# Optimization experiments

Hardware: AMD Instinct MI355X
Metric: run time of the kernel (lower is better)

Reference implementation:

```python
import jax, jax.numpy as jnp
import numpy as np

K = 2  # number of propagation hops (SGConv K)
NEG_SLOPE = 0.1


def setup_inputs() -> dict:
    key = jax.random.key(0)
    k1, k2, k3, k4 = jax.random.split(key, 4)
    N, E, C_in, C_out = 50000, 800000, 128, 512
    x = jax.random.normal(k1, (N, C_in), dtype=jnp.float32)
    edge_index = jax.random.randint(k2, (2, E), 0, N, dtype=jnp.int64)
    W = jax.random.normal(k3, (C_out, C_in), dtype=jnp.float32) * (1.0 / np.sqrt(C_in))
    b = jax.random.normal(k4, (C_out,), dtype=jnp.float32) * 0.01
    return {"x": x, "edge_index": edge_index, "W": W, "b": b}


def reference(x, edge_index, W, b):
    N = x.shape[0]
    # gcn_norm with self-loops (PyG SGConv default: add_self_loops=True)
    loop = jnp.arange(N, dtype=edge_index.dtype)
    src = jnp.concatenate([edge_index[0], loop])  # message sources j
    dst = jnp.concatenate([edge_index[1], loop])  # aggregation targets i
    deg = jax.ops.segment_sum(jnp.ones_like(dst, dtype=x.dtype), dst, num_segments=N)
    dinv = jnp.where(deg > 0, jax.lax.rsqrt(deg), 0.0)
    norm = dinv[src] * dinv[dst]  # [E+N]
    h = x
    for _ in range(K):
        h = jax.ops.segment_sum(norm[:, None] * h[src], dst, num_segments=N)
    y = h @ W.T + b
    return jnp.where(y >= 0, y, NEG_SLOPE * y)  # LeakyReLU(0.1)
```

## Files before the change

### kernel.cpp

```cpp
#include <hip/hip_runtime.h>
#include <hip/hip_bf16.h>

#define CIN 128
#define COUT 512
#define NEG_SLOPE 0.1f

typedef __bf16 bf16x8 __attribute__((ext_vector_type(8)));
typedef float f32x4 __attribute__((ext_vector_type(4)));

static __device__ __forceinline__ unsigned short f2bf(float f) {
  unsigned int u = __builtin_bit_cast(unsigned int, f);
  unsigned int lsb = (u >> 16) & 1u;
  u += 0x7fffu + lsb;
  return (unsigned short)(u >> 16);
}
static __device__ __forceinline__ float bf_lo(unsigned int u) {
  return __builtin_bit_cast(float, u << 16);
}
static __device__ __forceinline__ float bf_hi(unsigned int u) {
  return __builtin_bit_cast(float, u & 0xffff0000u);
}
static __device__ __forceinline__ unsigned int pack2(float lo, float hi) {
  return (unsigned int)f2bf(lo) | ((unsigned int)f2bf(hi) << 16);
}

__global__ void decode_count_kernel(const int* __restrict__ raw,
                                    int* __restrict__ srcA, int* __restrict__ dstA,
                                    int* __restrict__ rank, int* __restrict__ cnt,
                                    int E, int N) {
  __shared__ int s_is32;
  if (threadIdx.x == 0) s_is32 = 0;
  __syncthreads();
  int e = blockIdx.x * blockDim.x + threadIdx.x;
  int probe = 0;
  if (e < E) probe = raw[2 * e + 1];
  if (probe != 0) s_is32 = 1;
  __syncthreads();
  if (e >= E) return;
  int s, d;
  if (!s_is32) {
    int2 sv = ((const int2*)raw)[e];
    int2 dv = ((const int2*)raw)[E + e];
    s = sv.x;
    d = dv.x;
  } else {
    s = raw[e];
    d = raw[E + e];
  }
  if ((unsigned)s >= (unsigned)N) s = 0;
  if ((unsigned)d >= (unsigned)N) d = 0;
  srcA[e] = s;
  dstA[e] = d;
  rank[e] = atomicAdd(&cnt[d], 1);
}

__global__ __launch_bounds__(256) void scan_kernel(const int* __restrict__ cnt,
                                                   int* __restrict__ rowptr,
                                                   int* __restrict__ gcur, int N) {
  __shared__ int buf[256];
  __shared__ int sbase;
  int tid = threadIdx.x;
  int base = blockIdx.x * 1024 + tid * 4;
  int v[4];
  int tot = 0;
#pragma unroll
  for (int k = 0; k < 4; ++k) {
    int i = base + k;
    v[k] = (i < N) ? cnt[i] : 0;
    tot += v[k];
  }
  buf[tid] = tot;
  __syncthreads();
  for (int off = 1; off < 256; off <<= 1) {
    int t = (tid >= off) ? buf[tid - off] : 0;
    __syncthreads();
    buf[tid] += t;
    __syncthreads();
  }
  if (tid == 255) sbase = atomicAdd(gcur, buf[255]);
  __syncthreads();
  int run = sbase + buf[tid] - tot;
#pragma unroll
  for (int k = 0; k < 4; ++k) {
    int i = base + k;
    if (i < N) rowptr[i] = run;
    run += v[k];
  }
}

__global__ __launch_bounds__(256) void scatter_prep_kernel(
    const int* __restrict__ srcA, const int* __restrict__ dstA,
    const int* __restrict__ rank, const int* __restrict__ rowptr,
    int* __restrict__ col, int E,
    const float* __restrict__ x, const int* __restrict__ cnt,
    unsigned short* __restrict__ xs,
    const float* __restrict__ W, unsigned short* __restrict__ Wbf, int N) {
  int idx = blockIdx.x * blockDim.x + threadIdx.x;
  if (idx < E) {
    int d = dstA[idx];
    col[rowptr[d] + rank[idx]] = srcA[idx];
  }
  int nx = N * (CIN / 4);
  if (idx < nx) {
    int row = idx >> 5;
    float d = 1.0f / sqrtf((float)(cnt[row] + 1));
    float4 v = ((const float4*)x)[idx];
    ushort4 o;
    o.x = f2bf(v.x * d); o.y = f2bf(v.y * d); o.z = f2bf(v.z * d); o.w = f2bf(v.w * d);
    ((ushort4*)xs)[idx] = o;
  } else {
    int t = idx - nx;
    if (t < (COUT * CIN / 8)) {
      int lane = t & 63;
      int kk = (t >> 6) & 3;
      int nt = (t >> 8) & 7;
      int wv = t >> 11;
      int row = wv * 128 + nt * 16 + (lane & 15);
      int c = kk * 32 + (lane >> 4) * 8;
      const float* src = W + (size_t)row * CIN + c;
      float4 v0 = *(const float4*)src;
      float4 v1 = *(const float4*)(src + 4);
      ushort4 o0, o1;
      o0.x = f2bf(v0.x); o0.y = f2bf(v0.y); o0.z = f2bf(v0.z); o0.w = f2bf(v0.w);
      o1.x = f2bf(v1.x); o1.y = f2bf(v1.y); o1.z = f2bf(v1.z); o1.w = f2bf(v1.w);
      ((ushort4*)Wbf)[2 * t] = o0;
      ((ushort4*)Wbf)[2 * t + 1] = o1;
    }
  }
}

template <bool SQ>
__global__ __launch_bounds__(256) void hop_kernel(
    const unsigned short* __restrict__ Xs,
    const int* __restrict__ rowptr, const int* __restrict__ cnt,
    const int* __restrict__ col, unsigned short* __restrict__ Y, int N) {
  int lane = threadIdx.x & 63;
  int wid = threadIdx.x >> 6;
  int node = blockIdx.x * 4 + wid;
  if (node >= N) return;
  int sub = lane & 15;
  int grp = lane >> 4;
  int beg = rowptr[node];
  int num = cnt[node];
  const uint4* X4 = (const uint4*)Xs;
  float acc[8] = {0.f, 0.f, 0.f, 0.f, 0.f, 0.f, 0.f, 0.f};
  if (grp == 0) {
    uint4 s = X4[(size_t)node * 16 + sub];
    acc[0] = bf_lo(s.x); acc[1] = bf_hi(s.x);
    acc[2] = bf_lo(s.y); acc[3] = bf_hi(s.y);
    acc[4] = bf_lo(s.z); acc[5] = bf_hi(s.z);
    acc[6] = bf_lo(s.w); acc[7] = bf_hi(s.w);
  }
  const int* cp = col + beg;
  int kb = 0;
  for (; kb + 16 <= num; kb += 16) {
    int j0 = cp[kb + grp];
    int j1 = cp[kb + 4 + grp];
    int j2 = cp[kb + 8 + grp];
    int j3 = cp[kb + 12 + grp];
    uint4 v0 = X4[(size_t)j0 * 16 + sub];
    uint4 v1 = X4[(size_t)j1 * 16 + sub];
    uint4 v2 = X4[(size_t)j2 * 16 + sub];
    uint4 v3 = X4[(size_t)j3 * 16 + sub];
    acc[0] += bf_lo(v0.x); acc[1] += bf_hi(v0.x);
    acc[2] += bf_lo(v0.y); acc[3] += bf_hi(v0.y);
    acc[4] += bf_lo(v0.z); acc[5] += bf_hi(v0.z);
    acc[6] += bf_lo(v0.w); acc[7] += bf_hi(v0.w);
    acc[0] += bf_lo(v1.x); acc[1] += bf_hi(v1.x);
    acc[2] += bf_lo(v1.y); acc[3] += bf_hi(v1.y);
    acc[4] += bf_lo(v1.z); acc[5] += bf_hi(v1.z);
    acc[6] += bf_lo(v1.w); acc[7] += bf_hi(v1.w);
    acc[0] += bf_lo(v2.x); acc[1] += bf_hi(v2.x);
    acc[2] += bf_lo(v2.y); acc[3] += bf_hi(v2.y);
    acc[4] += bf_lo(v2.z); acc[5] += bf_hi(v2.z);
    acc[6] += bf_lo(v2.w); acc[7] += bf_hi(v2.w);
    acc[0] += bf_lo(v3.x); acc[1] += bf_hi(v3.x);
    acc[2] += bf_lo(v3.y); acc[3] += bf_hi(v3.y);
    acc[4] += bf_lo(v3.z); acc[5] += bf_hi(v3.z);
    acc[6] += bf_lo(v3.w); acc[7] += bf_hi(v3.w);
  }
  int rem = num - kb;
  if (rem >= 8) {
    int j0 = cp[kb + grp];
    int j1 = cp[kb + 4 + grp];
    uint4 v0 = X4[(size_t)j0 * 16 + sub];
    uint4 v1 = X4[(size_t)j1 * 16 + sub];
    acc[0] += bf_lo(v0.x); acc[1] += bf_hi(v0.x);
    acc[2] += bf_lo(v0.y); acc[3] += bf_hi(v0.y);
    acc[4] += bf_lo(v0.z); acc[5] += bf_hi(v0.z);
    acc[6] += bf_lo(v0.w); acc[7] += bf_hi(v0.w);
    acc[0] += bf_lo(v1.x); acc[1] += bf_hi(v1.x);
    acc[2] += bf_lo(v1.y); acc[3] += bf_hi(v1.y);
    acc[4] += bf_lo(v1.z); acc[5] += bf_hi(v1.z);
    acc[6] += bf_lo(v1.w); acc[7] += bf_hi(v1.w);
    kb += 8; rem -= 8;
  }
  if (rem >= 4) {
    int j0 = cp[kb + grp];
    uint4 v0 = X4[(size_t)j0 * 16 + sub];
    acc[0] += bf_lo(v0.x); acc[1] += bf_hi(v0.x);
    acc[2] += bf_lo(v0.y); acc[3] += bf_hi(v0.y);
    acc[4] += bf_lo(v0.z); acc[5] += bf_hi(v0.z);
    acc[6] += bf_lo(v0.w); acc[7] += bf_hi(v0.w);
    kb += 4; rem -= 4;
  }
  if (grp < rem) {
    int j0 = cp[kb + grp];
    uint4 v0 = X4[(size_t)j0 * 16 + sub];
    acc[0] += bf_lo(v0.x); acc[1] += bf_hi(v0.x);
    acc[2] += bf_lo(v0.y); acc[3] += bf_hi(v0.y);
    acc[4] += bf_lo(v0.z); acc[5] += bf_hi(v0.z);
    acc[6] += bf_lo(v0.w); acc[7] += bf_hi(v0.w);
  }
#pragma unroll
  for (int r = 0; r < 8; ++r) acc[r] += __shfl_xor(acc[r], 16, 64);
#pragma unroll
  for (int r = 0; r < 8; ++r) acc[r] += __shfl_xor(acc[r], 32, 64);
  if (grp == 0) {
    float di = 1.0f / sqrtf((float)(num + 1));
    float sc = SQ ? di * di : di;
    uint4 o;
    o.x = pack2(acc[0] * sc, acc[1] * sc);
    o.y = pack2(acc[2] * sc, acc[3] * sc);
    o.z = pack2(acc[4] * sc, acc[5] * sc);
    o.w = pack2(acc[6] * sc, acc[7] * sc);
    ((uint4*)Y)[(size_t)node * 16 + sub] = o;
  }
}

__global__ __launch_bounds__(256) void gemm_kernel(
    const unsigned short* __restrict__ Abf, const unsigned short* __restrict__ Wbf,
    const float* __restrict__ bias, float* __restrict__ out, int M) {
  __shared__ float tile[16 * 516];
  int wave = threadIdx.x >> 6;
  int lane = threadIdx.x & 63;
  int quad = lane >> 4;
  int l16 = lane & 15;
  int mbase = blockIdx.x * 32;

  int m0 = mbase + l16;
  int m1 = mbase + 16 + l16;
  bool v0 = m0 < M;
  bool v1 = m1 < M;

  bf16x8 af[2][4];
#pragma unroll
  for (int kk = 0; kk < 4; ++kk) {
    af[0][kk] = v0 ? *(const bf16x8*)(Abf + (size_t)m0 * CIN + kk * 32 + quad * 8) : bf16x8{};
    af[1][kk] = v1 ? *(const bf16x8*)(Abf + (size_t)m1 * CIN + kk * 32 + quad * 8) : bf16x8{};
  }

  const bf16x8* Wf = (const bf16x8*)Wbf;
  int nbase = wave * 128;
  f32x4 acc0[8], acc1[8];
#pragma unroll
  for (int nt = 0; nt < 8; ++nt) {
    bf16x8 wf[4];
#pragma unroll
    for (int kk = 0; kk < 4; ++kk)
      wf[kk] = Wf[(((wave * 8 + nt) * 4 + kk) << 6) + lane];
    f32x4 a0 = {}, a1 = {};
#pragma unroll
    for (int kk = 0; kk < 4; ++kk) {
      a0 = __builtin_amdgcn_mfma_f32_16x16x32_bf16(wf[kk], af[0][kk], a0, 0, 0, 0);
      a1 = __builtin_amdgcn_mfma_f32_16x16x32_bf16(wf[kk], af[1][kk], a1, 0, 0, 0);
    }
    acc0[nt] = a0;
    acc1[nt] = a1;
  }

#pragma unroll
  for (int half = 0; half < 2; ++half) {
    if (half) __syncthreads();
#pragma unroll
    for (int nt = 0; nt < 8; ++nt) {
      int n0 = nbase + nt * 16 + quad * 4;
      float4 bv = *(const float4*)(bias + n0);
      f32x4 a = half ? acc1[nt] : acc0[nt];
      float4 o;
      o.x = a[0] + bv.x; o.x = (o.x >= 0.f) ? o.x : NEG_SLOPE * o.x;
      o.y = a[1] + bv.y; o.y = (o.y >= 0.f) ? o.y : NEG_SLOPE * o.y;
      o.z = a[2] + bv.z; o.z = (o.z >= 0.f) ? o.z : NEG_SLOPE * o.z;
      o.w = a[3] + bv.w; o.w = (o.w >= 0.f) ? o.w : NEG_SLOPE * o.w;
      *(float4*)&tile[l16 * 516 + n0] = o;
    }
    __syncthreads();
#pragma unroll
    for (int it = 0; it < 8; ++it) {
      int r = it * 2 + (threadIdx.x >> 7);
      int c = (threadIdx.x & 127) * 4;
      int m = mbase + half * 16 + r;
      if (m < M) *(float4*)(out + (size_t)m * COUT + c) = *(const float4*)&tile[r * 516 + c];
    }
  }
}

static inline size_t align_up(size_t v, size_t a) { return (v + a - 1) & ~(a - 1); }

extern "C" void kernel_launch(void* const* d_in, const int* in_sizes, int n_in,
                              void* d_out, int out_size, void* d_ws, size_t ws_size,
                              hipStream_t stream) {
  const float* x = (const float*)d_in[0];
  const int* edge_raw = (const int*)d_in[1];
  const float* W = (const float*)d_in[2];
  const float* b = (const float*)d_in[3];
  float* out = (float*)d_out;

  const int N = in_sizes[0] / CIN;
  const int E = in_sizes[1] / 2;
  const int NB = (N + 1023) / 1024;

  char* w = (char*)d_ws;
  int* gcur = (int*)w;            w += 256;
  int* cnt = (int*)w;             w += align_up((size_t)N * 4, 256);
  int* rowptr = (int*)w;          w += align_up((size_t)N * 4, 256);
  int* srcA = (int*)w;            w += align_up((size_t)E * 4, 256);
  int* dstA = (int*)w;            w += align_up((size_t)E * 4, 256);
  int* rank = (int*)w;            w += align_up((size_t)E * 4, 256);
  int* col = (int*)w;             w += align_up((size_t)E * 4, 256);
  unsigned short* h2bf = (unsigned short*)w;  w += align_up((size_t)N * CIN * 2, 256);
  unsigned short* Wbf = (unsigned short*)w;   w += align_up((size_t)COUT * CIN * 2, 256);

  size_t outb = (size_t)out_size * sizeof(float);
  size_t rowb = (size_t)N * CIN * sizeof(unsigned short);
  unsigned short* h1s = (unsigned short*)((char*)d_out + (outb - rowb));
  unsigned short* xs = (unsigned short*)((char*)d_out + (outb - 2 * rowb));

  hipMemsetAsync(gcur, 0, 256 + (size_t)N * sizeof(int), stream);

  decode_count_kernel<<<(E + 255) / 256, 256, 0, stream>>>(edge_raw, srcA, dstA, rank, cnt, E, N);
  scan_kernel<<<NB, 256, 0, stream>>>(cnt, rowptr, gcur, N);

  int prep_elems = N * (CIN / 4) + COUT * CIN / 8;
  int sp_threads = (E > prep_elems) ? E : prep_elems;
  scatter_prep_kernel<<<(sp_threads + 255) / 256, 256, 0, stream>>>(
      srcA, dstA, rank, rowptr, col, E, x, cnt, xs, W, Wbf, N);

  hop_kernel<true><<<(N + 3) / 4, 256, 0, stream>>>(xs, rowptr, cnt, col, h1s, N);
  hop_kernel<false><<<(N + 3) / 4, 256, 0, stream>>>(h1s, rowptr, cnt, col, h2bf, N);

  gemm_kernel<<<(N + 31) / 32, 256, 0, stream>>>(h2bf, Wbf, b, out, N);
}
```

Baseline: 266.0 us.

## Fuse second propagation hop into GEMM kernel via shared-memory tile

The second SpMM hop now runs inside the GEMM kernel. Each block aggregates its 32 destination rows into a shared-memory bf16 tile, then feeds that tile straight to the MFMA loop. This drops one kernel launch and the write and re-read of the h2 intermediate in global memory. In exchange each GEMM block runs a serial gather over 8 nodes per wave before its matrix work, with fewer blocks (N/32) in flight for the gather phase, and h1 moves from the output buffer into workspace.

```diff
diff --git a/kernel.cpp b/kernel.cpp
--- a/kernel.cpp
+++ b/kernel.cpp
@@ -129,8 +129,7 @@
   }
 }
 
-template <bool SQ>
-__global__ __launch_bounds__(256) void hop_kernel(
+__global__ __launch_bounds__(256) void hop1_kernel(
     const unsigned short* __restrict__ Xs,
     const int* __restrict__ rowptr, const int* __restrict__ cnt,
     const int* __restrict__ col, unsigned short* __restrict__ Y, int N) {
@@ -218,7 +217,7 @@
   for (int r = 0; r < 8; ++r) acc[r] += __shfl_xor(acc[r], 32, 64);
   if (grp == 0) {
     float di = 1.0f / sqrtf((float)(num + 1));
-    float sc = SQ ? di * di : di;
+    float sc = di * di;
     uint4 o;
     o.x = pack2(acc[0] * sc, acc[1] * sc);
     o.y = pack2(acc[2] * sc, acc[3] * sc);
@@ -228,26 +227,122 @@
   }
 }
 
-__global__ __launch_bounds__(256) void gemm_kernel(
-    const unsigned short* __restrict__ Abf, const unsigned short* __restrict__ Wbf,
-    const float* __restrict__ bias, float* __restrict__ out, int M) {
-  __shared__ float tile[16 * 516];
+__global__ __launch_bounds__(256) void hopgemm_kernel(
+    const unsigned short* __restrict__ Xs,
+    const int* __restrict__ rowptr, const int* __restrict__ cnt,
+    const int* __restrict__ col,
+    const unsigned short* __restrict__ Wbf, const float* __restrict__ bias,
+    float* __restrict__ out, int N) {
+  __shared__ char smem[16 * 516 * 4];
+  unsigned short* s_h2 = (unsigned short*)smem;
+  float* tile = (float*)smem;
+
+  int lane = threadIdx.x & 63;
   int wave = threadIdx.x >> 6;
-  int lane = threadIdx.x & 63;
-  int quad = lane >> 4;
-  int l16 = lane & 15;
+  int sub = lane & 15;
+  int grp = lane >> 4;
   int mbase = blockIdx.x * 32;
-
-  int m0 = mbase + l16;
-  int m1 = mbase + 16 + l16;
-  bool v0 = m0 < M;
-  bool v1 = m1 < M;
-
+  const uint4* X4 = (const uint4*)Xs;
+
+  for (int t = 0; t < 8; ++t) {
+    int nl = wave * 8 + t;
+    int node = mbase + nl;
+    int beg = 0, num = 0;
+    if (node < N) { beg = rowptr[node]; num = cnt[node]; }
+    float acc[8] = {0.f, 0.f, 0.f, 0.f, 0.f, 0.f, 0.f, 0.f};
+    if (grp == 0 && node < N) {
+      uint4 s = X4[(size_t)node * 16 + sub];
+      acc[0] = bf_lo(s.x); acc[1] = bf_hi(s.x);
+      acc[2] = bf_lo(s.y); acc[3] = bf_hi(s.y);
+      acc[4] = bf_lo(s.z); acc[5] = bf_hi(s.z);
+      acc[6] = bf_lo(s.w); acc[7] = bf_hi(s.w);
+    }
+    const int* cp = col + beg;
+    int kb = 0;
+    for (; kb + 16 <= num; kb += 16) {
+      int j0 = cp[kb + grp];
+      int j1 = cp[kb + 4 + grp];
+      int j2 = cp[kb + 8 + grp];
+      int j3 = cp[kb + 12 + grp];
+      uint4 v0 = X4[(size_t)j0 * 16 + sub];
+      uint4 v1 = X4[(size_t)j1 * 16 + sub];
+      uint4 v2 = X4[(size_t)j2 * 16 + sub];
+      uint4 v3 = X4[(size_t)j3 * 16 + sub];
+      acc[0] += bf_lo(v0.x); acc[1] += bf_hi(v0.x);
+      acc[2] += bf_lo(v0.y); acc[3] += bf_hi(v0.y);
+      acc[4] += bf_lo(v0.z); acc[5] += bf_hi(v0.z);
+      acc[6] += bf_lo(v0.w); acc[7] += bf_hi(v0.w);
+      acc[0] += bf_lo(v1.x); acc[1] += bf_hi(v1.x);
+      acc[2] += bf_lo(v1.y); acc[3] += bf_hi(v1.y);
+      acc[4] += bf_lo(v1.z); acc[5] += bf_hi(v1.z);
+      acc[6] += bf_lo(v1.w); acc[7] += bf_hi(v1.w);
+      acc[0] += bf_lo(v2.x); acc[1] += bf_hi(v2.x);
+      acc[2] += bf_lo(v2.y); acc[3] += bf_hi(v2.y);
+      acc[4] += bf_lo(v2.z); acc[5] += bf_hi(v2.z);
+      acc[6] += bf_lo(v2.w); acc[7] += bf_hi(v2.w);
+      acc[0] += bf_lo(v3.x); acc[1] += bf_hi(v3.x);
+      acc[2] += bf_lo(v3.y); acc[3] += bf_hi(v3.y);
+      acc[4] += bf_lo(v3.z); acc[5] += bf_hi(v3.z);
+      acc[6] += bf_lo(v3.w); acc[7] += bf_hi(v3.w);
+    }
+    int rem = num - kb;
+    if (rem >= 8) {
+      int j0 = cp[kb + grp];
+      int j1 = cp[kb + 4 + grp];
+      uint4 v0 = X4[(size_t)j0 * 16 + sub];
+      uint4 v1 = X4[(size_t)j1 * 16 + sub];
+      acc[0] += bf_lo(v0.x); acc[1] += bf_hi(v0.x);
+      acc[2] += bf_lo(v0.y); acc[3] += bf_hi(v0.y);
+      acc[4] += bf_lo(v0.z); acc[5] += bf_hi(v0.z);
+      acc[6] += bf_lo(v0.w); acc[7] += bf_hi(v0.w);
+      acc[0] += bf_lo(v1.x); acc[1] += bf_hi(v1.x);
+      acc[2] += bf_lo(v1.y); acc[3] += bf_hi(v1.y);
+      acc[4] += bf_lo(v1.z); acc[5] += bf_hi(v1.z);
+      acc[6] += bf_lo(v1.w); acc[7] += bf_hi(v1.w);
+      kb += 8; rem -= 8;
+    }
+    if (rem >= 4) {
+      int j0 = cp[kb + grp];
+      uint4 v0 = X4[(size_t)j0 * 16 + sub];
+      acc[0] += bf_lo(v0.x); acc[1] += bf_hi(v0.x);
+      acc[2] += bf_lo(v0.y); acc[3] += bf_hi(v0.y);
+      acc[4] += bf_lo(v0.z); acc[5] += bf_hi(v0.z);
+      acc[6] += bf_lo(v0.w); acc[7] += bf_hi(v0.w);
+      kb += 4; rem -= 4;
+    }
+    if (grp < rem) {
+      int j0 = cp[kb + grp];
+      uint4 v0 = X4[(size_t)j0 * 16 + sub];
+      acc[0] += bf_lo(v0.x); acc[1] += bf_hi(v0.x);
+      acc[2] += bf_lo(v0.y); acc[3] += bf_hi(v0.y);
+      acc[4] += bf_lo(v0.z); acc[5] += bf_hi(v0.z);
+      acc[6] += bf_lo(v0.w); acc[7] += bf_hi(v0.w);
+    }
+#pragma unroll
+    for (int r = 0; r < 8; ++r) acc[r] += __shfl_xor(acc[r], 16, 64);
+#pragma unroll
+    for (int r = 0; r < 8; ++r) acc[r] += __shfl_xor(acc[r], 32, 64);
+    if (grp == 0) {
+      uint4 o = {0u, 0u, 0u, 0u};
+      if (node < N) {
+        float di = 1.0f / sqrtf((float)(num + 1));
+        o.x = pack2(acc[0] * di, acc[1] * di);
+        o.y = pack2(acc[2] * di, acc[3] * di);
+        o.z = pack2(acc[4] * di, acc[5] * di);
+        o.w = pack2(acc[6] * di, acc[7] * di);
+      }
+      *(uint4*)&s_h2[nl * 136 + sub * 8] = o;
+    }
+  }
+  __syncthreads();
+
+  int quad = grp;
+  int l16 = sub;
   bf16x8 af[2][4];
 #pragma unroll
   for (int kk = 0; kk < 4; ++kk) {
-    af[0][kk] = v0 ? *(const bf16x8*)(Abf + (size_t)m0 * CIN + kk * 32 + quad * 8) : bf16x8{};
-    af[1][kk] = v1 ? *(const bf16x8*)(Abf + (size_t)m1 * CIN + kk * 32 + quad * 8) : bf16x8{};
+    af[0][kk] = *(const bf16x8*)&s_h2[l16 * 136 + kk * 32 + quad * 8];
+    af[1][kk] = *(const bf16x8*)&s_h2[(16 + l16) * 136 + kk * 32 + quad * 8];
   }
 
   const bf16x8* Wf = (const bf16x8*)Wbf;
@@ -268,6 +363,7 @@
     acc0[nt] = a0;
     acc1[nt] = a1;
   }
+  __syncthreads();
 
 #pragma unroll
   for (int half = 0; half < 2; ++half) {
@@ -290,7 +386,7 @@
       int r = it * 2 + (threadIdx.x >> 7);
       int c = (threadIdx.x & 127) * 4;
       int m = mbase + half * 16 + r;
-      if (m < M) *(float4*)(out + (size_t)m * COUT + c) = *(const float4*)&tile[r * 516 + c];
+      if (m < N) *(float4*)(out + (size_t)m * COUT + c) = *(const float4*)&tile[r * 516 + c];
     }
   }
 }
@@ -318,13 +414,12 @@
   int* dstA = (int*)w;            w += align_up((size_t)E * 4, 256);
   int* rank = (int*)w;            w += align_up((size_t)E * 4, 256);
   int* col = (int*)w;             w += align_up((size_t)E * 4, 256);
-  unsigned short* h2bf = (unsigned short*)w;  w += align_up((size_t)N * CIN * 2, 256);
+  unsigned short* h1s = (unsigned short*)w;   w += align_up((size_t)N * CIN * 2, 256);
   unsigned short* Wbf = (unsigned short*)w;   w += align_up((size_t)COUT * CIN * 2, 256);
 
   size_t outb = (size_t)out_size * sizeof(float);
   size_t rowb = (size_t)N * CIN * sizeof(unsigned short);
-  unsigned short* h1s = (unsigned short*)((char*)d_out + (outb - rowb));
-  unsigned short* xs = (unsigned short*)((char*)d_out + (outb - 2 * rowb));
+  unsigned short* xs = (unsigned short*)((char*)d_out + (outb - rowb));
 
   hipMemsetAsync(gcur, 0, 256 + (size_t)N * sizeof(int), stream);
 
@@ -336,8 +431,7 @@
   scatter_prep_kernel<<<(sp_threads + 255) / 256, 256, 0, stream>>>(
       srcA, dstA, rank, rowptr, col, E, x, cnt, xs, W, Wbf, N);
 
-  hop_kernel<true><<<(N + 3) / 4, 256, 0, stream>>>(xs, rowptr, cnt, col, h1s, N);
-  hop_kernel<false><<<(N + 3) / 4, 256, 0, stream>>>(h1s, rowptr, cnt, col, h2bf, N);
-
-  gemm_kernel<<<(N + 31) / 32, 256, 0, stream>>>(h2bf, Wbf, b, out, N);
-}
+  hop1_kernel<<<(N + 3) / 4, 256, 0, stream>>>(xs, rowptr, cnt, col, h1s, N);
+
+  hopgemm_kernel<<<(N + 31) / 32, 256, 0, stream>>>(h1s, rowptr, cnt, col, Wbf, b, out, N);
+}
```

Measured after the change: 287.9 us. +8.2%, slower.

## Slice features into channel chunks so per-hop gathers stay L2-resident

Applied to the files above, without the earlier changes.

Stores the scaled input and hop outputs in a slice-major layout of four 32-channel chunks and runs both propagation hops separately per slice. The intent is to shrink the random-gather working set so neighbor rows hit in cache instead of HBM. In exchange, edge index lists are reread four times, each gather fetches only 64 bytes, the unrolled multi-load loop is replaced by a simple single-load loop, and the number of kernel launches grows.

```diff
diff --git a/kernel.cpp b/kernel.cpp
--- a/kernel.cpp
+++ b/kernel.cpp
@@ -100,14 +100,21 @@
     int d = dstA[idx];
     col[rowptr[d] + rank[idx]] = srcA[idx];
   }
-  int nx = N * (CIN / 4);
+  int nx = N * 16;
   if (idx < nx) {
-    int row = idx >> 5;
-    float d = 1.0f / sqrtf((float)(cnt[row] + 1));
-    float4 v = ((const float4*)x)[idx];
-    ushort4 o;
-    o.x = f2bf(v.x * d); o.y = f2bf(v.y * d); o.z = f2bf(v.z * d); o.w = f2bf(v.w * d);
-    ((ushort4*)xs)[idx] = o;
+    int node = idx >> 4;
+    int part = idx & 15;
+    int slice = part >> 2;
+    float d = 1.0f / sqrtf((float)(cnt[node] + 1));
+    const float* src = x + (size_t)node * CIN + part * 8;
+    float4 v0 = *(const float4*)src;
+    float4 v1 = *(const float4*)(src + 4);
+    uint4 o;
+    o.x = pack2(v0.x * d, v0.y * d);
+    o.y = pack2(v0.z * d, v0.w * d);
+    o.z = pack2(v1.x * d, v1.y * d);
+    o.w = pack2(v1.z * d, v1.w * d);
+    *(uint4*)&xs[((size_t)slice * N + node) * 32 + (part & 3) * 8] = o;
   } else {
     int t = idx - nx;
     if (t < (COUT * CIN / 8)) {
@@ -130,7 +137,7 @@
 }
 
 template <bool SQ>
-__global__ __launch_bounds__(256) void hop_kernel(
+__global__ __launch_bounds__(256) void hop_slice_kernel(
     const unsigned short* __restrict__ Xs,
     const int* __restrict__ rowptr, const int* __restrict__ cnt,
     const int* __restrict__ col, unsigned short* __restrict__ Y, int N) {
@@ -138,80 +145,35 @@
   int wid = threadIdx.x >> 6;
   int node = blockIdx.x * 4 + wid;
   if (node >= N) return;
-  int sub = lane & 15;
-  int grp = lane >> 4;
+  int sub = lane & 3;
+  int grp = lane >> 2;
   int beg = rowptr[node];
   int num = cnt[node];
   const uint4* X4 = (const uint4*)Xs;
   float acc[8] = {0.f, 0.f, 0.f, 0.f, 0.f, 0.f, 0.f, 0.f};
   if (grp == 0) {
-    uint4 s = X4[(size_t)node * 16 + sub];
+    uint4 s = X4[(size_t)node * 4 + sub];
     acc[0] = bf_lo(s.x); acc[1] = bf_hi(s.x);
     acc[2] = bf_lo(s.y); acc[3] = bf_hi(s.y);
     acc[4] = bf_lo(s.z); acc[5] = bf_hi(s.z);
     acc[6] = bf_lo(s.w); acc[7] = bf_hi(s.w);
   }
   const int* cp = col + beg;
-  int kb = 0;
-  for (; kb + 16 <= num; kb += 16) {
-    int j0 = cp[kb + grp];
-    int j1 = cp[kb + 4 + grp];
-    int j2 = cp[kb + 8 + grp];
-    int j3 = cp[kb + 12 + grp];
-    uint4 v0 = X4[(size_t)j0 * 16 + sub];
-    uint4 v1 = X4[(size_t)j1 * 16 + sub];
-    uint4 v2 = X4[(size_t)j2 * 16 + sub];
-    uint4 v3 = X4[(size_t)j3 * 16 + sub];
-    acc[0] += bf_lo(v0.x); acc[1] += bf_hi(v0.x);
-    acc[2] += bf_lo(v0.y); acc[3] += bf_hi(v0.y);
-    acc[4] += bf_lo(v0.z); acc[5] += bf_hi(v0.z);
-    acc[6] += bf_lo(v0.w); acc[7] += bf_hi(v0.w);
-    acc[0] += bf_lo(v1.x); acc[1] += bf_hi(v1.x);
-    acc[2] += bf_lo(v1.y); acc[3] += bf_hi(v1.y);
-    acc[4] += bf_lo(v1.z); acc[5] += bf_hi(v1.z);
-    acc[6] += bf_lo(v1.w); acc[7] += bf_hi(v1.w);
-    acc[0] += bf_lo(v2.x); acc[1] += bf_hi(v2.x);
-    acc[2] += bf_lo(v2.y); acc[3] += bf_hi(v2.y);
-    acc[4] += bf_lo(v2.z); acc[5] += bf_hi(v2.z);
-    acc[6] += bf_lo(v2.w); acc[7] += bf_hi(v2.w);
-    acc[0] += bf_lo(v3.x); acc[1] += bf_hi(v3.x);
-    acc[2] += bf_lo(v3.y); acc[3] += bf_hi(v3.y);
-    acc[4] += bf_lo(v3.z); acc[5] += bf_hi(v3.z);
-    acc[6] += bf_lo(v3.w); acc[7] += bf_hi(v3.w);
-  }
-  int rem = num - kb;
-  if (rem >= 8) {
-    int j0 = cp[kb + grp];
-    int j1 = cp[kb + 4 + grp];
-    uint4 v0 = X4[(size_t)j0 * 16 + sub];
-    uint4 v1 = X4[(size_t)j1 * 16 + sub];
-    acc[0] += bf_lo(v0.x); acc[1] += bf_hi(v0.x);
-    acc[2] += bf_lo(v0.y); acc[3] += bf_hi(v0.y);
-    acc[4] += bf_lo(v0.z); acc[5] += bf_hi(v0.z);
-    acc[6] += bf_lo(v0.w); acc[7] += bf_hi(v0.w);
-    acc[0] += bf_lo(v1.x); acc[1] += bf_hi(v1.x);
-    acc[2] += bf_lo(v1.y); acc[3] += bf_hi(v1.y);
-    acc[4] += bf_lo(v1.z); acc[5] += bf_hi(v1.z);
-    acc[6] += bf_lo(v1.w); acc[7] += bf_hi(v1.w);
-    kb += 8; rem -= 8;
-  }
-  if (rem >= 4) {
-    int j0 = cp[kb + grp];
-    uint4 v0 = X4[(size_t)j0 * 16 + sub];
-    acc[0] += bf_lo(v0.x); acc[1] += bf_hi(v0.x);
-    acc[2] += bf_lo(v0.y); acc[3] += bf_hi(v0.y);
-    acc[4] += bf_lo(v0.z); acc[5] += bf_hi(v0.z);
-    acc[6] += bf_lo(v0.w); acc[7] += bf_hi(v0.w);
-    kb += 4; rem -= 4;
-  }
-  if (grp < rem) {
-    int j0 = cp[kb + grp];
-    uint4 v0 = X4[(size_t)j0 * 16 + sub];
-    acc[0] += bf_lo(v0.x); acc[1] += bf_hi(v0.x);
-    acc[2] += bf_lo(v0.y); acc[3] += bf_hi(v0.y);
-    acc[4] += bf_lo(v0.z); acc[5] += bf_hi(v0.z);
-    acc[6] += bf_lo(v0.w); acc[7] += bf_hi(v0.w);
-  }
+  for (int kb = 0; kb < num; kb += 16) {
+    int k = kb + grp;
+    if (k < num) {
+      int j = cp[k];
+      uint4 v = X4[(size_t)j * 4 + sub];
+      acc[0] += bf_lo(v.x); acc[1] += bf_hi(v.x);
+      acc[2] += bf_lo(v.y); acc[3] += bf_hi(v.y);
+      acc[4] += bf_lo(v.z); acc[5] += bf_hi(v.z);
+      acc[6] += bf_lo(v.w); acc[7] += bf_hi(v.w);
+    }
+  }
+#pragma unroll
+  for (int r = 0; r < 8; ++r) acc[r] += __shfl_xor(acc[r], 4, 64);
+#pragma unroll
+  for (int r = 0; r < 8; ++r) acc[r] += __shfl_xor(acc[r], 8, 64);
 #pragma unroll
   for (int r = 0; r < 8; ++r) acc[r] += __shfl_xor(acc[r], 16, 64);
 #pragma unroll
@@ -224,7 +186,7 @@
     o.y = pack2(acc[2] * sc, acc[3] * sc);
     o.z = pack2(acc[4] * sc, acc[5] * sc);
     o.w = pack2(acc[6] * sc, acc[7] * sc);
-    ((uint4*)Y)[(size_t)node * 16 + sub] = o;
+    ((uint4*)Y)[(size_t)node * 4 + sub] = o;
   }
 }
 
@@ -246,8 +208,8 @@
   bf16x8 af[2][4];
 #pragma unroll
   for (int kk = 0; kk < 4; ++kk) {
-    af[0][kk] = v0 ? *(const bf16x8*)(Abf + (size_t)m0 * CIN + kk * 32 + quad * 8) : bf16x8{};
-    af[1][kk] = v1 ? *(const bf16x8*)(Abf + (size_t)m1 * CIN + kk * 32 + quad * 8) : bf16x8{};
+    af[0][kk] = v0 ? *(const bf16x8*)(Abf + ((size_t)kk * M + m0) * 32 + quad * 8) : bf16x8{};
+    af[1][kk] = v1 ? *(const bf16x8*)(Abf + ((size_t)kk * M + m1) * 32 + quad * 8) : bf16x8{};
   }
 
   const bf16x8* Wf = (const bf16x8*)Wbf;
@@ -318,26 +280,31 @@
   int* dstA = (int*)w;            w += align_up((size_t)E * 4, 256);
   int* rank = (int*)w;            w += align_up((size_t)E * 4, 256);
   int* col = (int*)w;             w += align_up((size_t)E * 4, 256);
-  unsigned short* h2bf = (unsigned short*)w;  w += align_up((size_t)N * CIN * 2, 256);
+  unsigned short* h1 = (unsigned short*)w;    w += align_up((size_t)N * 32 * 2, 256);
+  unsigned short* h2 = (unsigned short*)w;    w += align_up((size_t)N * CIN * 2, 256);
   unsigned short* Wbf = (unsigned short*)w;   w += align_up((size_t)COUT * CIN * 2, 256);
 
   size_t outb = (size_t)out_size * sizeof(float);
   size_t rowb = (size_t)N * CIN * sizeof(unsigned short);
-  unsigned short* h1s = (unsigned short*)((char*)d_out + (outb - rowb));
-  unsigned short* xs = (unsigned short*)((char*)d_out + (outb - 2 * rowb));
+  unsigned short* xs = (unsigned short*)((char*)d_out + (outb - rowb));
 
   hipMemsetAsync(gcur, 0, 256 + (size_t)N * sizeof(int), stream);
 
   decode_count_kernel<<<(E + 255) / 256, 256, 0, stream>>>(edge_raw, srcA, dstA, rank, cnt, E, N);
   scan_kernel<<<NB, 256, 0, stream>>>(cnt, rowptr, gcur, N);
 
-  int prep_elems = N * (CIN / 4) + COUT * CIN / 8;
+  int prep_elems = N * 16 + COUT * CIN / 8;
   int sp_threads = (E > prep_elems) ? E : prep_elems;
   scatter_prep_kernel<<<(sp_threads + 255) / 256, 256, 0, stream>>>(
       srcA, dstA, rank, rowptr, col, E, x, cnt, xs, W, Wbf, N);
 
-  hop_kernel<true><<<(N + 3) / 4, 256, 0, stream>>>(xs, rowptr, cnt, col, h1s, N);
-  hop_kernel<false><<<(N + 3) / 4, 256, 0, stream>>>(h1s, rowptr, cnt, col, h2bf, N);
-
-  gemm_kernel<<<(N + 31) / 32, 256, 0, stream>>>(h2bf, Wbf, b, out, N);
-}
+  int hop_blocks = (N + 3) / 4;
+  for (int s = 0; s < 4; ++s) {
+    unsigned short* xs_s = xs + (size_t)s * N * 32;
+    unsigned short* h2_s = h2 + (size_t)s * N * 32;
+    hop_slice_kernel<true><<<hop_blocks, 256, 0, stream>>>(xs_s, rowptr, cnt, col, h1, N);
+    hop_slice_kernel<false><<<hop_blocks, 256, 0, stream>>>(h1, rowptr, cnt, col, h2_s, N);
+  }
+
+  gemm_kernel<<<(N + 31) / 32, 256, 0, stream>>>(h2, Wbf, b, out, N);
+}
```

Result: slower. 369.9 us (+39.0%).
